# Kernel optimization log

Measured on AMD Instinct MI355X. Metric: run time of the kernel, lower is better.

## Reference

```python
import jax, jax.numpy as jnp
import numpy as np

B, N, DIM = 4, 2048, 512
H, DH = 8, 64  # heads, dim_head; inner_dim = H*DH = 512
SCALE = DH ** -0.5
EPS = 1e-5


def _layer_norm(x, gamma):
    # LayerNorm with learned gamma and beta fixed to zeros (beta is a buffer)
    mu = jnp.mean(x, axis=-1, keepdims=True)
    var = jnp.var(x, axis=-1, keepdims=True)
    return (x - mu) * jax.lax.rsqrt(var + EPS) * gamma


def setup_inputs() -> dict:
    key = jax.random.key(0)
    ks = jax.random.split(key, 6)
    x = jax.random.normal(ks[0], (B, N, DIM), jnp.float32)
    mask = jax.random.bernoulli(ks[1], 0.9, (B, N))  # bool [b, n]
    gamma = jnp.ones((DIM,), jnp.float32)            # pre-attn LayerNorm gamma
    Wq = jax.random.normal(ks[2], (DIM, H * DH), jnp.float32) * 0.02
    Wkv = jax.random.normal(ks[3], (DIM, 2 * DH), jnp.float32) * 0.02  # shared single KV head (MQA)
    null_kv = jax.random.normal(ks[4], (2, DH), jnp.float32)
    Wout = jax.random.normal(ks[5], (H * DH, DIM), jnp.float32) * 0.02
    out_gamma = jnp.ones((DIM,), jnp.float32)        # post-proj LayerNorm gamma
    return {"x": x, "mask": mask, "gamma": gamma, "Wq": Wq, "Wkv": Wkv,
            "null_kv": null_kv, "Wout": Wout, "out_gamma": out_gamma}


def reference(x, mask, gamma, Wq, Wkv, null_kv, Wout, out_gamma):
    b, n, _ = x.shape
    xn = _layer_norm(x, gamma)
    # queries: per-head; keys/values: single shared head (multi-query)
    q = (xn @ Wq).reshape(b, n, H, DH).transpose(0, 2, 1, 3) * SCALE  # [b,h,n,d]
    kv = xn @ Wkv                                                     # [b,n,2d]
    k, v = kv[..., :DH], kv[..., DH:]                                 # [b,n,d]
    # prepend learned null key/value (attention sink) shared across batch
    nk = jnp.broadcast_to(null_kv[0], (b, 1, DH))
    nv = jnp.broadcast_to(null_kv[1], (b, 1, DH))
    k = jnp.concatenate([nk, k], axis=1)  # [b, n+1, d]
    v = jnp.concatenate([nv, v], axis=1)
    sim = jnp.einsum('bhid,bjd->bhij', q, k)  # [b,h,n,n+1]
    # mask padded with True for the null token, broadcast over heads/queries
    m = jnp.concatenate([jnp.ones((b, 1), bool), mask], axis=1)
    max_neg = -jnp.finfo(sim.dtype).max
    sim = jnp.where(m[:, None, None, :], sim, max_neg)
    attn = jax.nn.softmax(sim.astype(jnp.float32), axis=-1).astype(x.dtype)
    out = jnp.einsum('bhij,bjd->bhid', attn, v)       # [b,h,n,d]
    out = out.transpose(0, 2, 1, 3).reshape(b, n, H * DH)
    return _layer_norm(out @ Wout, out_gamma)
```

## Files before the change

kernel.cpp:

```cpp
#include <hip/hip_runtime.h>

typedef __attribute__((ext_vector_type(8)))  short bf16x8;
typedef __attribute__((ext_vector_type(4)))  float f32x4;
typedef __attribute__((ext_vector_type(16))) float f32x16;
typedef __attribute__((ext_vector_type(4)))  unsigned u32x4;

#define Nx 2048
#define CTXx 2049
#define KCAP 2112
#define QSCALE 0.18033688f

__device__ __forceinline__ short f2bs(float x){
    unsigned u = __builtin_bit_cast(unsigned, x);
    u = (u + 0x7fffu + ((u >> 16) & 1u)) >> 16;
    return (short)u;
}
__device__ __forceinline__ unsigned pack_trunc(float a, float b){
    return __builtin_amdgcn_perm(__builtin_bit_cast(unsigned, b),
                                 __builtin_bit_cast(unsigned, a), 0x07060302u);
}

__global__ void __launch_bounds__(256) ln1_prep_kernel(const float* __restrict__ x,
                                                       const float* __restrict__ g,
                                                       short* __restrict__ xnb,
                                                       const float* __restrict__ Wq,
                                                       const float* __restrict__ Wkv,
                                                       const float* __restrict__ Wout,
                                                       const float* __restrict__ nkv,
                                                       short* __restrict__ WcatT,
                                                       short* __restrict__ WoutT,
                                                       short* __restrict__ kb,
                                                       short* __restrict__ vbt){
    __shared__ float ls[64][65];
    int t = threadIdx.x;
    if (blockIdx.x < 2048){
        int w = t >> 6, lane = t & 63;
        size_t row = (size_t)blockIdx.x * 4 + w;
        const float* xr = x + row * 512 + lane * 8;
        float4 a = *(const float4*)xr;
        float4 b = *(const float4*)(xr + 4);
        float s = a.x + a.y + a.z + a.w + b.x + b.y + b.z + b.w;
        float q = a.x*a.x + a.y*a.y + a.z*a.z + a.w*a.w
                + b.x*b.x + b.y*b.y + b.z*b.z + b.w*b.w;
        #pragma unroll
        for (int m = 1; m < 64; m <<= 1){ s += __shfl_xor(s, m, 64); q += __shfl_xor(q, m, 64); }
        float mu  = s * (1.f / 512.f);
        float var = fmaxf(q * (1.f / 512.f) - mu * mu, 0.f);
        float r   = rsqrtf(var + 1e-5f);
        const float* gr = g + lane * 8;
        float4 g0 = *(const float4*)gr;
        float4 g1 = *(const float4*)(gr + 4);
        bf16x8 o;
        o[0] = f2bs((a.x - mu) * r * g0.x); o[1] = f2bs((a.y - mu) * r * g0.y);
        o[2] = f2bs((a.z - mu) * r * g0.z); o[3] = f2bs((a.w - mu) * r * g0.w);
        o[4] = f2bs((b.x - mu) * r * g1.x); o[5] = f2bs((b.y - mu) * r * g1.y);
        o[6] = f2bs((b.z - mu) * r * g1.z); o[7] = f2bs((b.w - mu) * r * g1.w);
        *(bf16x8*)(xnb + row * 512 + lane * 8) = o;
        return;
    }
    int bid = blockIdx.x - 2048;
    if (bid == 144){
        int b = t >> 6, d = t & 63;
        kb[((size_t)b * KCAP) * 64 + d] = f2bs(nkv[d]);
        vbt[((size_t)b * 64 + d) * KCAP + 0] = f2bs(nkv[64 + d]);
        return;
    }
    bool isOut = (bid >= 80);
    int b2 = isOut ? bid - 80 : bid;
    int ntile = isOut ? (b2 & 7) : (b2 % 10);
    int ktile = isOut ? (b2 >> 3) : (b2 / 10);
    int n0 = ntile * 64, k0 = ktile * 64;
    #pragma unroll
    for (int rr = 0; rr < 64; rr += 16){
        int r = rr + (t >> 4), c = (t & 15) * 4;
        float4 v;
        if (isOut)            v = *(const float4*)(Wout + (size_t)(k0 + r) * 512 + n0 + c);
        else if (n0 < 512)    v = *(const float4*)(Wq   + (size_t)(k0 + r) * 512 + n0 + c);
        else                  v = *(const float4*)(Wkv  + (size_t)(k0 + r) * 128 + (n0 - 512) + c);
        ls[c + 0][r] = v.x; ls[c + 1][r] = v.y; ls[c + 2][r] = v.z; ls[c + 3][r] = v.w;
    }
    __syncthreads();
    int rn = t >> 2, kc = (t & 3) * 16;
    short tmp[16];
    #pragma unroll
    for (int j = 0; j < 16; j++) tmp[j] = f2bs(ls[rn][kc + j]);
    short* dst = (isOut ? WoutT : WcatT) + (size_t)(n0 + rn) * 512 + k0 + kc;
    *(int4*)dst       = *(int4*)&tmp[0];
    *(int4*)(dst + 8) = *(int4*)&tmp[8];
}

__global__ void __launch_bounds__(256, 1) gemm_qkv(const short* __restrict__ A,
                                                   const short* __restrict__ BwT,
                                                   short* __restrict__ qb,
                                                   short* __restrict__ kb,
                                                   short* __restrict__ vbt){
    int t = threadIdx.x, lane = t & 63, w = t >> 6;
    int l16 = lane & 15, quad = lane >> 4;
    int row0 = blockIdx.x * 32;
    const short* aB = A   + (size_t)(row0 + l16) * 512 + quad * 8;
    const short* bB = BwT + (size_t)(w * 160 + l16) * 512 + quad * 8;
    f32x4 acc[2][10];
    #pragma unroll
    for (int mt = 0; mt < 2; mt++)
        #pragma unroll
        for (int nt = 0; nt < 10; nt++) acc[mt][nt] = (f32x4){0.f, 0.f, 0.f, 0.f};
    bf16x8 af[2][2], bf[2][10];
    #pragma unroll
    for (int mt = 0; mt < 2; mt++) af[0][mt] = *(const bf16x8*)(aB + mt * 8192);
    #pragma unroll
    for (int nt = 0; nt < 10; nt++) bf[0][nt] = *(const bf16x8*)(bB + nt * 8192);
    #pragma unroll
    for (int it = 0; it < 16; ++it){
        int cur = it & 1, nxt = cur ^ 1;
        if (it < 15){
            int kn = (it + 1) * 32;
            #pragma unroll
            for (int mt = 0; mt < 2; mt++) af[nxt][mt] = *(const bf16x8*)(aB + mt * 8192 + kn);
            #pragma unroll
            for (int nt = 0; nt < 10; nt++) bf[nxt][nt] = *(const bf16x8*)(bB + nt * 8192 + kn);
        }
        #pragma unroll
        for (int mt = 0; mt < 2; mt++)
            #pragma unroll
            for (int nt = 0; nt < 10; nt++)
                acc[mt][nt] = __builtin_amdgcn_mfma_f32_16x16x32_bf16(af[cur][mt], bf[cur][nt], acc[mt][nt], 0, 0, 0);
    }
    #pragma unroll
    for (int mt = 0; mt < 2; mt++)
        #pragma unroll
        for (int nt = 0; nt < 10; nt++)
            #pragma unroll
            for (int r = 0; r < 4; r++){
                int row = row0 + mt * 16 + quad * 4 + r;
                int col = w * 160 + nt * 16 + l16;
                float v = acc[mt][nt][r];
                int bb = row >> 11, ii = row & 2047;
                if (col < 512){
                    qb[(size_t)row * 512 + col] = f2bs(v * QSCALE);
                } else if (col < 576){
                    kb[((size_t)bb * KCAP + ii + 1) * 64 + (col - 512)] = f2bs(v);
                } else {
                    vbt[((size_t)bb * 64 + (col - 576)) * KCAP + ii + 1] = f2bs(v);
                }
            }
}

__global__ void __launch_bounds__(256, 1) gemm_out_ln2(const short* __restrict__ A,
                                                       const short* __restrict__ BwT,
                                                       const float* __restrict__ og,
                                                       float* __restrict__ out){
    __shared__ float Sred[4][32], Qred[4][32];
    int t = threadIdx.x, lane = t & 63, w = t >> 6;
    int l16 = lane & 15, quad = lane >> 4;
    int row0 = blockIdx.x * 32;
    const short* aB = A   + (size_t)(row0 + l16) * 512 + quad * 8;
    const short* bB = BwT + (size_t)(w * 128 + l16) * 512 + quad * 8;
    f32x4 acc[2][8];
    #pragma unroll
    for (int mt = 0; mt < 2; mt++)
        #pragma unroll
        for (int nt = 0; nt < 8; nt++) acc[mt][nt] = (f32x4){0.f, 0.f, 0.f, 0.f};
    bf16x8 af[2][2], bf[2][8];
    #pragma unroll
    for (int mt = 0; mt < 2; mt++) af[0][mt] = *(const bf16x8*)(aB + mt * 8192);
    #pragma unroll
    for (int nt = 0; nt < 8; nt++) bf[0][nt] = *(const bf16x8*)(bB + nt * 8192);
    #pragma unroll
    for (int it = 0; it < 16; ++it){
        int cur = it & 1, nxt = cur ^ 1;
        if (it < 15){
            int kn = (it + 1) * 32;
            #pragma unroll
            for (int mt = 0; mt < 2; mt++) af[nxt][mt] = *(const bf16x8*)(aB + mt * 8192 + kn);
            #pragma unroll
            for (int nt = 0; nt < 8; nt++) bf[nxt][nt] = *(const bf16x8*)(bB + nt * 8192 + kn);
        }
        #pragma unroll
        for (int mt = 0; mt < 2; mt++)
            #pragma unroll
            for (int nt = 0; nt < 8; nt++)
                acc[mt][nt] = __builtin_amdgcn_mfma_f32_16x16x32_bf16(af[cur][mt], bf[cur][nt], acc[mt][nt], 0, 0, 0);
    }
    #pragma unroll
    for (int mt = 0; mt < 2; mt++)
        #pragma unroll
        for (int r = 0; r < 4; r++){
            float s = 0.f, q = 0.f;
            #pragma unroll
            for (int nt = 0; nt < 8; nt++){
                float v = acc[mt][nt][r];
                s += v; q += v * v;
            }
            #pragma unroll
            for (int m = 1; m < 16; m <<= 1){ s += __shfl_xor(s, m, 64); q += __shfl_xor(q, m, 64); }
            if (l16 == 0){
                int rl = mt * 16 + quad * 4 + r;
                Sred[w][rl] = s; Qred[w][rl] = q;
            }
        }
    __syncthreads();
    #pragma unroll
    for (int mt = 0; mt < 2; mt++)
        #pragma unroll
        for (int r = 0; r < 4; r++){
            int rl = mt * 16 + quad * 4 + r;
            float S = Sred[0][rl] + Sred[1][rl] + Sred[2][rl] + Sred[3][rl];
            float Q = Qred[0][rl] + Qred[1][rl] + Qred[2][rl] + Qred[3][rl];
            float mu  = S * (1.f / 512.f);
            float var = fmaxf(Q * (1.f / 512.f) - mu * mu, 0.f);
            float rstd = rsqrtf(var + 1e-5f);
            float* op = out + (size_t)(row0 + rl) * 512;
            #pragma unroll
            for (int nt = 0; nt < 8; nt++){
                int col = w * 128 + nt * 16 + l16;
                op[col] = (acc[mt][nt][r] - mu) * rstd * og[col];
            }
        }
}

__global__ void __launch_bounds__(256, 2) attn_kernel(const short* __restrict__ qb,
                                                      const short* __restrict__ kb,
                                                      const short* __restrict__ vbt,
                                                      const int* __restrict__ mask,
                                                      short* __restrict__ ob){
    __shared__ short Ks[2][64][72];
    __shared__ short Vt[2][64][72];
    int t = threadIdx.x;
    int lane = t & 63, w = t >> 6;
    int n32 = lane & 31, hb = lane >> 5;
    int b = blockIdx.y, i0 = blockIdx.x * 16;
    int head = 2 * w + (n32 >> 4), row = i0 + (n32 & 15);
    bf16x8 qf[4];
    {
        const short* qp = qb + ((size_t)(b * Nx + row)) * 512 + head * 64 + hb * 8;
        #pragma unroll
        for (int ks = 0; ks < 4; ks++) qf[ks] = *(const bf16x8*)(qp + ks * 16);
    }
    bf16x8 ones;
    #pragma unroll
    for (int j = 0; j < 8; j++) ones[j] = (short)0x3F80;
    f32x16 oacc[2], lacc;
    #pragma unroll
    for (int j = 0; j < 16; j++){ oacc[0][j] = 0.f; oacc[1][j] = 0.f; lacc[j] = 0.f; }

    int skey = t >> 2, sd = (t & 3) * 16;
    int vd   = t >> 2, vk = (t & 3) * 16;
    const short* kgp = kb  + (size_t)b * KCAP * 64 + skey * 64 + sd;
    const short* vgp = vbt + ((size_t)b * 64 + vd) * KCAP + vk;
    const int* mrow = mask + b * Nx;

    int4 pk0 = *(const int4*)(kgp);
    int4 pk1 = *(const int4*)(kgp + 8);
    int4 pv0 = *(const int4*)(vgp);
    int4 pv1 = *(const int4*)(vgp + 8);
    int mok = (lane == 0) ? 1 : ((lane < CTXx) ? mrow[lane - 1] : 0);

    int p = 0;
    for (int jt = 0; jt < 33; ++jt){
        *(int4*)&Ks[p][skey][sd]     = pk0;
        *(int4*)&Ks[p][skey][sd + 8] = pk1;
        *(int4*)&Vt[p][vd][vk]       = make_int4(pv0.x, pv0.y, pv1.x, pv1.y);
        *(int4*)&Vt[p][vd][vk + 8]   = make_int4(pv0.z, pv0.w, pv1.z, pv1.w);
        unsigned long long bal = __ballot(mok != 0);
        __syncthreads();
        int jn = (jt + 1) * 64;
        if (jt + 1 < 33){
            pk0 = *(const int4*)(kgp + (size_t)jn * 64);
            pk1 = *(const int4*)(kgp + (size_t)jn * 64 + 8);
            pv0 = *(const int4*)(vgp + jn);
            pv1 = *(const int4*)(vgp + jn + 8);
            int jg = jn + lane;
            mok = (jg < CTXx) ? mrow[jg - 1] : 0;
        }
        f32x16 sf[2];
        #pragma unroll
        for (int i = 0; i < 2; i++)
            #pragma unroll
            for (int j = 0; j < 16; j++) sf[i][j] = 0.f;
        #pragma unroll
        for (int ks = 0; ks < 4; ks++){
            #pragma unroll
            for (int kt = 0; kt < 2; kt++){
                bf16x8 kf = *(const bf16x8*)&Ks[p][kt * 32 + n32][ks * 16 + hb * 8];
                sf[kt] = __builtin_amdgcn_mfma_f32_32x32x16_bf16(kf, qf[ks], sf[kt], 0, 0, 0);
            }
        }
        unsigned mlo = (unsigned)(bal >> (4 * hb));
        unsigned mhi = (unsigned)(bal >> (32 + 4 * hb));
        unsigned pg[8][2];
        #pragma unroll
        for (int kt = 0; kt < 2; kt++){
            unsigned mm = kt ? mhi : mlo;
            #pragma unroll
            for (int g4 = 0; g4 < 4; g4++){
                float pr[4];
                #pragma unroll
                for (int tt = 0; tt < 4; tt++){
                    float e = __builtin_amdgcn_exp2f(sf[kt][g4 * 4 + tt]);
                    pr[tt] = ((mm >> (8 * g4 + tt)) & 1u) ? e : 0.f;
                }
                pg[kt * 4 + g4][0] = pack_trunc(pr[0], pr[1]);
                pg[kt * 4 + g4][1] = pack_trunc(pr[2], pr[3]);
            }
        }
        #pragma unroll
        for (int s = 0; s < 4; s++){
            bf16x8 pa = __builtin_bit_cast(bf16x8,
                (u32x4){pg[2 * s][0], pg[2 * s][1], pg[2 * s + 1][0], pg[2 * s + 1][1]});
            lacc = __builtin_amdgcn_mfma_f32_32x32x16_bf16(pa, ones, lacc, 0, 0, 0);
            #pragma unroll
            for (int nt = 0; nt < 2; nt++){
                bf16x8 vf = *(const bf16x8*)&Vt[p][nt * 32 + n32][s * 16 + hb * 8];
                oacc[nt] = __builtin_amdgcn_mfma_f32_32x32x16_bf16(pa, vf, oacc[nt], 0, 0, 0);
            }
        }
        p ^= 1;
    }
    #pragma unroll
    for (int r = 0; r < 16; r++){
        float linv = 1.f / lacc[r];
        int hr = (r & 3) + 8 * (r >> 2) + 4 * hb;
        int grow = i0 + (hr & 15);
        int ghead = 2 * w + (hr >> 4);
        short* op = ob + ((size_t)(b * Nx + grow)) * 512 + ghead * 64 + n32;
        op[0]  = f2bs(oacc[0][r] * linv);
        op[32] = f2bs(oacc[1][r] * linv);
    }
}

extern "C" void kernel_launch(void* const* d_in, const int* in_sizes, int n_in,
                              void* d_out, int out_size, void* d_ws, size_t ws_size,
                              hipStream_t stream){
    const float* x     = (const float*)d_in[0];
    const int*   mask  = (const int*)  d_in[1];
    const float* gamma = (const float*)d_in[2];
    const float* Wq    = (const float*)d_in[3];
    const float* Wkv   = (const float*)d_in[4];
    const float* nkv   = (const float*)d_in[5];
    const float* Wout  = (const float*)d_in[6];
    const float* og    = (const float*)d_in[7];
    float* out = (float*)d_out;

    short* xnb   = (short*)d_ws;
    short* qb    = xnb + (size_t)4194304;
    short* kb    = qb  + (size_t)4194304;
    short* vbt   = kb  + (size_t)540672;
    short* WcatT = vbt + (size_t)540672;
    short* WoutT = WcatT + (size_t)327680;
    short* ob    = xnb;

    ln1_prep_kernel<<<2193, 256, 0, stream>>>(x, gamma, xnb, Wq, Wkv, Wout, nkv,
                                              WcatT, WoutT, kb, vbt);
    gemm_qkv    <<<256, 256, 0, stream>>>(xnb, WcatT, qb, kb, vbt);
    attn_kernel <<<dim3(128, 4), 256, 0, stream>>>(qb, kb, vbt, mask, ob);
    gemm_out_ln2<<<256, 256, 0, stream>>>(ob, WoutT, og, out);
}
```

Baseline: 182.4 us.

## Process two 16-row query tiles per attention block to reuse K/V tiles

Each attention workgroup now handles 32 query rows (two row tiles) instead of 16, so each K/V tile staged in shared memory and each LDS fragment read feeds twice as many MFMAs. The grid halves to 64x4 blocks and launch bounds drop to one block per SIMD group, allowing more registers for the doubled accumulators. The cost is fewer workgroups (256 on a large GPU), lower occupancy and higher register pressure, which may reduce latency hiding.

```diff
diff --git a/kernel.cpp b/kernel.cpp
--- a/kernel.cpp
+++ b/kernel.cpp
@@ -218,7 +218,7 @@
         }
 }
 
-__global__ void __launch_bounds__(256, 2) attn_kernel(const short* __restrict__ qb,
+__global__ void __launch_bounds__(256, 1) attn_kernel(const short* __restrict__ qb,
                                                       const short* __restrict__ kb,
                                                       const short* __restrict__ vbt,
                                                       const int* __restrict__ mask,
@@ -228,20 +228,25 @@
     int t = threadIdx.x;
     int lane = t & 63, w = t >> 6;
     int n32 = lane & 31, hb = lane >> 5;
-    int b = blockIdx.y, i0 = blockIdx.x * 16;
-    int head = 2 * w + (n32 >> 4), row = i0 + (n32 & 15);
-    bf16x8 qf[4];
-    {
+    int b = blockIdx.y, i0 = blockIdx.x * 32;
+    int head = 2 * w + (n32 >> 4);
+    bf16x8 qf[2][4];
+    #pragma unroll
+    for (int rt = 0; rt < 2; rt++){
+        int row = i0 + rt * 16 + (n32 & 15);
         const short* qp = qb + ((size_t)(b * Nx + row)) * 512 + head * 64 + hb * 8;
         #pragma unroll
-        for (int ks = 0; ks < 4; ks++) qf[ks] = *(const bf16x8*)(qp + ks * 16);
+        for (int ks = 0; ks < 4; ks++) qf[rt][ks] = *(const bf16x8*)(qp + ks * 16);
     }
     bf16x8 ones;
     #pragma unroll
     for (int j = 0; j < 8; j++) ones[j] = (short)0x3F80;
-    f32x16 oacc[2], lacc;
-    #pragma unroll
-    for (int j = 0; j < 16; j++){ oacc[0][j] = 0.f; oacc[1][j] = 0.f; lacc[j] = 0.f; }
+    f32x16 oacc[2][2], lacc[2];
+    #pragma unroll
+    for (int rt = 0; rt < 2; rt++){
+        #pragma unroll
+        for (int j = 0; j < 16; j++){ oacc[rt][0][j] = 0.f; oacc[rt][1][j] = 0.f; lacc[rt][j] = 0.f; }
+    }
 
     int skey = t >> 2, sd = (t & 3) * 16;
     int vd   = t >> 2, vk = (t & 3) * 16;
@@ -272,60 +277,69 @@
             int jg = jn + lane;
             mok = (jg < CTXx) ? mrow[jg - 1] : 0;
         }
-        f32x16 sf[2];
-        #pragma unroll
-        for (int i = 0; i < 2; i++)
-            #pragma unroll
-            for (int j = 0; j < 16; j++) sf[i][j] = 0.f;
+        f32x16 sf[2][2];
+        #pragma unroll
+        for (int rt = 0; rt < 2; rt++)
+            #pragma unroll
+            for (int kt = 0; kt < 2; kt++)
+                #pragma unroll
+                for (int j = 0; j < 16; j++) sf[rt][kt][j] = 0.f;
         #pragma unroll
         for (int ks = 0; ks < 4; ks++){
             #pragma unroll
             for (int kt = 0; kt < 2; kt++){
                 bf16x8 kf = *(const bf16x8*)&Ks[p][kt * 32 + n32][ks * 16 + hb * 8];
-                sf[kt] = __builtin_amdgcn_mfma_f32_32x32x16_bf16(kf, qf[ks], sf[kt], 0, 0, 0);
+                sf[0][kt] = __builtin_amdgcn_mfma_f32_32x32x16_bf16(kf, qf[0][ks], sf[0][kt], 0, 0, 0);
+                sf[1][kt] = __builtin_amdgcn_mfma_f32_32x32x16_bf16(kf, qf[1][ks], sf[1][kt], 0, 0, 0);
             }
         }
         unsigned mlo = (unsigned)(bal >> (4 * hb));
         unsigned mhi = (unsigned)(bal >> (32 + 4 * hb));
-        unsigned pg[8][2];
-        #pragma unroll
-        for (int kt = 0; kt < 2; kt++){
-            unsigned mm = kt ? mhi : mlo;
-            #pragma unroll
-            for (int g4 = 0; g4 < 4; g4++){
-                float pr[4];
+        unsigned pg[2][8][2];
+        #pragma unroll
+        for (int rt = 0; rt < 2; rt++)
+            #pragma unroll
+            for (int kt = 0; kt < 2; kt++){
+                unsigned mm = kt ? mhi : mlo;
                 #pragma unroll
-                for (int tt = 0; tt < 4; tt++){
-                    float e = __builtin_amdgcn_exp2f(sf[kt][g4 * 4 + tt]);
-                    pr[tt] = ((mm >> (8 * g4 + tt)) & 1u) ? e : 0.f;
+                for (int g4 = 0; g4 < 4; g4++){
+                    float pr[4];
+                    #pragma unroll
+                    for (int tt = 0; tt < 4; tt++){
+                        float e = __builtin_amdgcn_exp2f(sf[rt][kt][g4 * 4 + tt]);
+                        pr[tt] = ((mm >> (8 * g4 + tt)) & 1u) ? e : 0.f;
+                    }
+                    pg[rt][kt * 4 + g4][0] = pack_trunc(pr[0], pr[1]);
+                    pg[rt][kt * 4 + g4][1] = pack_trunc(pr[2], pr[3]);
                 }
-                pg[kt * 4 + g4][0] = pack_trunc(pr[0], pr[1]);
-                pg[kt * 4 + g4][1] = pack_trunc(pr[2], pr[3]);
-            }
-        }
+            }
         #pragma unroll
         for (int s = 0; s < 4; s++){
-            bf16x8 pa = __builtin_bit_cast(bf16x8,
-                (u32x4){pg[2 * s][0], pg[2 * s][1], pg[2 * s + 1][0], pg[2 * s + 1][1]});
-            lacc = __builtin_amdgcn_mfma_f32_32x32x16_bf16(pa, ones, lacc, 0, 0, 0);
-            #pragma unroll
-            for (int nt = 0; nt < 2; nt++){
-                bf16x8 vf = *(const bf16x8*)&Vt[p][nt * 32 + n32][s * 16 + hb * 8];
-                oacc[nt] = __builtin_amdgcn_mfma_f32_32x32x16_bf16(pa, vf, oacc[nt], 0, 0, 0);
+            bf16x8 vf0 = *(const bf16x8*)&Vt[p][n32][s * 16 + hb * 8];
+            bf16x8 vf1 = *(const bf16x8*)&Vt[p][32 + n32][s * 16 + hb * 8];
+            #pragma unroll
+            for (int rt = 0; rt < 2; rt++){
+                bf16x8 pa = __builtin_bit_cast(bf16x8,
+                    (u32x4){pg[rt][2 * s][0], pg[rt][2 * s][1], pg[rt][2 * s + 1][0], pg[rt][2 * s + 1][1]});
+                lacc[rt]    = __builtin_amdgcn_mfma_f32_32x32x16_bf16(pa, ones, lacc[rt], 0, 0, 0);
+                oacc[rt][0] = __builtin_amdgcn_mfma_f32_32x32x16_bf16(pa, vf0, oacc[rt][0], 0, 0, 0);
+                oacc[rt][1] = __builtin_amdgcn_mfma_f32_32x32x16_bf16(pa, vf1, oacc[rt][1], 0, 0, 0);
             }
         }
         p ^= 1;
     }
     #pragma unroll
-    for (int r = 0; r < 16; r++){
-        float linv = 1.f / lacc[r];
-        int hr = (r & 3) + 8 * (r >> 2) + 4 * hb;
-        int grow = i0 + (hr & 15);
-        int ghead = 2 * w + (hr >> 4);
-        short* op = ob + ((size_t)(b * Nx + grow)) * 512 + ghead * 64 + n32;
-        op[0]  = f2bs(oacc[0][r] * linv);
-        op[32] = f2bs(oacc[1][r] * linv);
-    }
+    for (int rt = 0; rt < 2; rt++)
+        #pragma unroll
+        for (int r = 0; r < 16; r++){
+            float linv = 1.f / lacc[rt][r];
+            int hr = (r & 3) + 8 * (r >> 2) + 4 * hb;
+            int grow = i0 + rt * 16 + (hr & 15);
+            int ghead = 2 * w + (hr >> 4);
+            short* op = ob + ((size_t)(b * Nx + grow)) * 512 + ghead * 64 + n32;
+            op[0]  = f2bs(oacc[rt][0][r] * linv);
+            op[32] = f2bs(oacc[rt][1][r] * linv);
+        }
 }
 
 extern "C" void kernel_launch(void* const* d_in, const int* in_sizes, int n_in,
@@ -352,6 +366,6 @@
     ln1_prep_kernel<<<2193, 256, 0, stream>>>(x, gamma, xnb, Wq, Wkv, Wout, nkv,
                                               WcatT, WoutT, kb, vbt);
     gemm_qkv    <<<256, 256, 0, stream>>>(xnb, WcatT, qb, kb, vbt);
-    attn_kernel <<<dim3(128, 4), 256, 0, stream>>>(qb, kb, vbt, mask, ob);
+    attn_kernel <<<dim3(64, 4), 256, 0, stream>>>(qb, kb, vbt, mask, ob);
     gemm_out_ln2<<<256, 256, 0, stream>>>(ob, WoutT, og, out);
 }
```

New measurement: 184.0 us. Within noise of the previous version (+0.9%).
